# Optimization experiments

Hardware: AMD Instinct MI355X
Metric: run time of the kernel (lower is better)

## Reference

```python
import jax, jax.numpy as jnp
import numpy as np


def _gru(x_seq, W_ih, W_hh, b_ih, b_hh):
    """Batched torch-style GRU. x_seq: [B,T,H] -> outputs [B,T,H].
    Gate order (torch.nn.GRU): r, z, n. n = tanh(xn + r*(W_hn h + b_hn))."""
    B, T, H = x_seq.shape
    # precompute input projections for all timesteps: [B,T,3H]
    xp = jnp.einsum('bth,gh->btg', x_seq, W_ih) + b_ih

    def step(h, xt):  # h: [B,H], xt: [B,3H]
        hp = h @ W_hh.T + b_hh  # [B,3H]
        xr, xz, xn = jnp.split(xt, 3, axis=-1)
        hr, hz, hn = jnp.split(hp, 3, axis=-1)
        r = jax.nn.sigmoid(xr + hr)
        z = jax.nn.sigmoid(xz + hz)
        n = jnp.tanh(xn + r * hn)
        h_new = (1.0 - z) * n + z * h
        return h_new, h_new

    h0 = jnp.zeros((B, H), dtype=x_seq.dtype)
    _, hs = jax.lax.scan(step, h0, jnp.swapaxes(xp, 0, 1))  # [T,B,H]
    return jnp.swapaxes(hs, 0, 1)


def setup_inputs() -> dict:
    key = jax.random.key(0)
    B, T, C, H, D = 128, 64, 8000, 256, 16
    G = 3 * H
    ks = jax.random.split(key, 32)
    s = 0.05  # scale for stable params
    inp = {
        'x': (jax.random.uniform(ks[0], (B, T, C)) < 0.01).astype(jnp.float32),  # sparse multi-hot
        'demographic': jax.random.normal(ks[1], (B, D), jnp.float32),
        'embed_W': jax.random.normal(ks[2], (H, C), jnp.float32) * s,
        'embed_b': jax.random.normal(ks[3], (H,), jnp.float32) * s,
        'aW_ih': jax.random.normal(ks[4], (G, H), jnp.float32) * s,
        'aW_hh': jax.random.normal(ks[5], (G, H), jnp.float32) * s,
        'ab_ih': jax.random.normal(ks[6], (G,), jnp.float32) * s,
        'ab_hh': jax.random.normal(ks[7], (G,), jnp.float32) * s,
        'bW_ih': jax.random.normal(ks[8], (G, H), jnp.float32) * s,
        'bW_hh': jax.random.normal(ks[9], (G, H), jnp.float32) * s,
        'bb_ih': jax.random.normal(ks[10], (G,), jnp.float32) * s,
        'bb_hh': jax.random.normal(ks[11], (G,), jnp.float32) * s,
        'attnA_W': jax.random.normal(ks[12], (1, H), jnp.float32) * s,
        'attnA_b': jax.random.normal(ks[13], (1,), jnp.float32) * s,
        'attnB_W': jax.random.normal(ks[14], (H, H), jnp.float32) * s,
        'attnB_b': jax.random.normal(ks[15], (H,), jnp.float32) * s,
        'cls_W1': jax.random.normal(ks[16], (H, H + D), jnp.float32) * s,
        'cls_b1': jax.random.normal(ks[17], (H,), jnp.float32) * s,
        'cls_W2': jax.random.normal(ks[18], (C, H), jnp.float32) * s,
        'cls_b2': jax.random.normal(ks[19], (C,), jnp.float32) * s,
        'dl_W1': jax.random.normal(ks[20], (H, H + D), jnp.float32) * s,
        'dl_b1': jax.random.normal(ks[21], (H,), jnp.float32) * s,
        'dl_W2': jax.random.normal(ks[22], (1, H), jnp.float32) * s,
        'dl_b2': jax.random.normal(ks[23], (1,), jnp.float32) * s,
    }
    return inp


def reference(x, demographic, embed_W, embed_b,
              aW_ih, aW_hh, ab_ih, ab_hh,
              bW_ih, bW_hh, bb_ih, bb_hh,
              attnA_W, attnA_b, attnB_W, attnB_b,
              cls_W1, cls_b1, cls_W2, cls_b2,
              dl_W1, dl_b1, dl_W2, dl_b2):
    # code embedding: [B,T,C] @ [C,H] -> [B,T,H]
    embedded = jnp.einsum('btc,hc->bth', x, embed_W) + embed_b

    alpha_out = _gru(embedded, aW_ih, aW_hh, ab_ih, ab_hh)  # [B,T,H]
    beta_out = _gru(embedded, bW_ih, bW_hh, bb_ih, bb_hh)   # [B,T,H]

    e_alpha = jnp.einsum('bth,oh->bto', alpha_out, attnA_W)[..., 0] + attnA_b[0]  # [B,T]
    alpha = jax.nn.softmax(e_alpha, axis=1)                                       # [B,T]
    beta = jnp.tanh(jnp.einsum('bth,gh->btg', beta_out, attnB_W) + attnB_b)       # [B,T,H]

    context = jnp.einsum('bth,bt->bh', embedded * beta, alpha)  # [B,H]

    combined = jnp.concatenate([context, demographic], axis=1)  # [B,H+D]
    # classifier (dropout = identity, eval mode)
    h1 = jax.nn.relu(combined @ cls_W1.T + cls_b1)
    logits = h1 @ cls_W2.T + cls_b2                              # [B,C]
    # death/LOS head
    h2 = jax.nn.relu(combined @ dl_W1.T + dl_b1)
    dl_logit = h2 @ dl_W2.T + dl_b2                              # [B,1]

    return jnp.concatenate([logits, dl_logit], axis=1)          # [B,C+1]
```

## Files before the change

kernel.cpp:

```cpp
#include <hip/hip_runtime.h>


typedef __attribute__((ext_vector_type(4))) float f32x4;
typedef __attribute__((ext_vector_type(8))) short short8;

__device__ inline short f2bf(float f) {
  unsigned u = __float_as_uint(f);
  u += 0x7fffu + ((u >> 16) & 1u);
  return (short)(u >> 16);
}
__device__ inline float sigf(float x) { return 1.f / (1.f + __expf(-x)); }
__device__ inline float tanh_fast(float x) {
  x = fminf(fmaxf(x, -15.f), 15.f);
  float e = __expf(2.f * x);
  return (e - 1.f) / (e + 1.f);
}

__global__ void transpose_w(const float* __restrict__ in, float* __restrict__ outT) {
  __shared__ float tile[32][33];
  const int tx = threadIdx.x, ty = threadIdx.y;
  const int c0 = blockIdx.x * 32, h0 = blockIdx.y * 32;
#pragma unroll
  for (int k = 0; k < 4; ++k)
    tile[ty * 4 + k][tx] = in[(long)(h0 + ty * 4 + k) * 8000 + c0 + tx];
  __syncthreads();
#pragma unroll
  for (int k = 0; k < 4; ++k)
    outT[(long)(c0 + ty * 4 + k) * 256 + h0 + tx] = tile[tx][ty * 4 + k];
}

__global__ __launch_bounds__(256) void pad_w1(const float* __restrict__ w1,
                                              const float* __restrict__ w1d,
                                              float* __restrict__ o1,
                                              float* __restrict__ o2) {
  int idx = blockIdx.x * 256 + threadIdx.x;
  if (idx >= 2 * 256 * 288) return;
  int half = idx / (256 * 288);
  int r = idx % (256 * 288);
  int n = r / 288, k = r % 288;
  float v = (k < 272) ? (half ? w1d[n * 272 + k] : w1[n * 272 + k]) : 0.f;
  if (half) o2[r] = v; else o1[r] = v;
}

__global__ __launch_bounds__(512) void pack_whh(const float* __restrict__ aWhh,
                                                const float* __restrict__ bWhh,
                                                short* __restrict__ wbf) {
  const int F = blockIdx.x * 512 + threadIdx.x;
  int f = F;
  const int lane = f & 63; f >>= 6;
  const int w = f & 15; f >>= 4;
  const int e = f % 3; f /= 3;
  const int kt = f & 7; f >>= 3;
  const int gru = f;
  const float* W = gru ? bWhh : aWhh;
  const int g = e * 256 + w * 16 + (lane & 15);
  const int k = kt * 32 + (lane >> 4) * 8;
  const float* p = W + (long)g * 256 + k;
  short8 v;
#pragma unroll
  for (int j = 0; j < 8; ++j) v[j] = f2bf(p[j]);
  *(short8*)(wbf + (long)F * 8) = v;
}

__global__ __launch_bounds__(256) void embed_sparse(const float* __restrict__ x,
                                                    const float* __restrict__ Wt,
                                                    const float* __restrict__ eb,
                                                    float* __restrict__ emb) {
  __shared__ int sidx[512];
  __shared__ float sval[512];
  __shared__ int scnt;
  const int bt = blockIdx.x;
  const int tid = threadIdx.x;
  if (tid == 0) scnt = 0;
  __syncthreads();
  const float* xr = x + (long)bt * 8000;
  for (int i = tid; i < 2000; i += 256) {
    float4 v = ((const float4*)xr)[i];
    if (v.x != 0.f) { int p = atomicAdd(&scnt, 1); if (p < 512) { sidx[p] = i * 4 + 0; sval[p] = v.x; } }
    if (v.y != 0.f) { int p = atomicAdd(&scnt, 1); if (p < 512) { sidx[p] = i * 4 + 1; sval[p] = v.y; } }
    if (v.z != 0.f) { int p = atomicAdd(&scnt, 1); if (p < 512) { sidx[p] = i * 4 + 2; sval[p] = v.z; } }
    if (v.w != 0.f) { int p = atomicAdd(&scnt, 1); if (p < 512) { sidx[p] = i * 4 + 3; sval[p] = v.w; } }
  }
  __syncthreads();
  const int n = min(scnt, 512);
  float acc = eb[tid];
  for (int i = 0; i < n; ++i) acc += sval[i] * Wt[(long)sidx[i] * 256 + tid];
  emb[(long)bt * 256 + tid] = acc;
}

__global__ __launch_bounds__(256) void gemm_bt(const float* __restrict__ A,
                                               const float* __restrict__ B,
                                               const float* __restrict__ bias,
                                               float* __restrict__ C,
                                               int M, int N, int K, int ldc, int act) {
  __shared__ short As[64][40];
  __shared__ short Bs[64][40];
  const int tid = threadIdx.x;
  const int lane = tid & 63, wave = tid >> 6;
  const int wm = wave >> 1, wn = wave & 1;
  const int l15 = lane & 15, lhi = lane >> 4;
  const int m0 = blockIdx.y * 64, n0 = blockIdx.x * 64;
  const int srow = tid >> 2, scol = (tid & 3) * 8;
  f32x4 acc[2][2];
#pragma unroll
  for (int i = 0; i < 2; ++i)
#pragma unroll
    for (int j = 0; j < 2; ++j) acc[i][j] = (f32x4){0.f, 0.f, 0.f, 0.f};

  for (int k0 = 0; k0 < K; k0 += 32) {
    __syncthreads();
    {
      const float* p = A + (long)(m0 + srow) * K + k0 + scol;
      float4 f0 = *(const float4*)p;
      float4 f1 = *(const float4*)(p + 4);
      short8 v;
      v[0] = f2bf(f0.x); v[1] = f2bf(f0.y); v[2] = f2bf(f0.z); v[3] = f2bf(f0.w);
      v[4] = f2bf(f1.x); v[5] = f2bf(f1.y); v[6] = f2bf(f1.z); v[7] = f2bf(f1.w);
      *(short8*)&As[srow][scol] = v;
      const float* q = B + (long)(n0 + srow) * K + k0 + scol;
      float4 g0 = *(const float4*)q;
      float4 g1 = *(const float4*)(q + 4);
      short8 u;
      u[0] = f2bf(g0.x); u[1] = f2bf(g0.y); u[2] = f2bf(g0.z); u[3] = f2bf(g0.w);
      u[4] = f2bf(g1.x); u[5] = f2bf(g1.y); u[6] = f2bf(g1.z); u[7] = f2bf(g1.w);
      *(short8*)&Bs[srow][scol] = u;
    }
    __syncthreads();
    short8 af0 = *(const short8*)&As[wm * 32 + l15][lhi * 8];
    short8 af1 = *(const short8*)&As[wm * 32 + 16 + l15][lhi * 8];
    short8 bf0 = *(const short8*)&Bs[wn * 32 + l15][lhi * 8];
    short8 bf1 = *(const short8*)&Bs[wn * 32 + 16 + l15][lhi * 8];
    acc[0][0] = __builtin_amdgcn_mfma_f32_16x16x32_bf16(af0, bf0, acc[0][0], 0, 0, 0);
    acc[0][1] = __builtin_amdgcn_mfma_f32_16x16x32_bf16(af0, bf1, acc[0][1], 0, 0, 0);
    acc[1][0] = __builtin_amdgcn_mfma_f32_16x16x32_bf16(af1, bf0, acc[1][0], 0, 0, 0);
    acc[1][1] = __builtin_amdgcn_mfma_f32_16x16x32_bf16(af1, bf1, acc[1][1], 0, 0, 0);
  }
#pragma unroll
  for (int j = 0; j < 2; ++j) {
    const int col = n0 + wn * 32 + j * 16 + l15;
    const float bv = bias[col];
#pragma unroll
    for (int i = 0; i < 2; ++i) {
#pragma unroll
      for (int r = 0; r < 4; ++r) {
        const int row = m0 + wm * 32 + i * 16 + lhi * 4 + r;
        float v = acc[i][j][r] + bv;
        if (act == 1) v = fmaxf(v, 0.f);
        else if (act == 2) v = tanh_fast(v);
        C[(long)row * ldc + col] = v;
      }
    }
  }
}

__global__ __launch_bounds__(256) void gemm_dual(const float* __restrict__ A,
                                                 const float* __restrict__ B1,
                                                 const float* __restrict__ B2,
                                                 const float* __restrict__ bias1,
                                                 const float* __restrict__ bias2,
                                                 float* __restrict__ C1,
                                                 float* __restrict__ C2,
                                                 int K) {
  __shared__ short As[64][40];
  __shared__ short Bs1[64][40];
  __shared__ short Bs2[64][40];
  const int tid = threadIdx.x;
  const int lane = tid & 63, wave = tid >> 6;
  const int wm = wave >> 1, wn = wave & 1;
  const int l15 = lane & 15, lhi = lane >> 4;
  const int m0 = blockIdx.y * 64, n0 = blockIdx.x * 64;
  const int srow = tid >> 2, scol = (tid & 3) * 8;
  f32x4 acc1[2][2], acc2[2][2];
#pragma unroll
  for (int i = 0; i < 2; ++i)
#pragma unroll
    for (int j = 0; j < 2; ++j) {
      acc1[i][j] = (f32x4){0.f, 0.f, 0.f, 0.f};
      acc2[i][j] = (f32x4){0.f, 0.f, 0.f, 0.f};
    }

  for (int k0 = 0; k0 < K; k0 += 32) {
    __syncthreads();
    {
      const float* p = A + (long)(m0 + srow) * K + k0 + scol;
      float4 f0 = *(const float4*)p;
      float4 f1 = *(const float4*)(p + 4);
      short8 v;
      v[0] = f2bf(f0.x); v[1] = f2bf(f0.y); v[2] = f2bf(f0.z); v[3] = f2bf(f0.w);
      v[4] = f2bf(f1.x); v[5] = f2bf(f1.y); v[6] = f2bf(f1.z); v[7] = f2bf(f1.w);
      *(short8*)&As[srow][scol] = v;
      const float* q1 = B1 + (long)(n0 + srow) * K + k0 + scol;
      float4 g0 = *(const float4*)q1;
      float4 g1 = *(const float4*)(q1 + 4);
      short8 u;
      u[0] = f2bf(g0.x); u[1] = f2bf(g0.y); u[2] = f2bf(g0.z); u[3] = f2bf(g0.w);
      u[4] = f2bf(g1.x); u[5] = f2bf(g1.y); u[6] = f2bf(g1.z); u[7] = f2bf(g1.w);
      *(short8*)&Bs1[srow][scol] = u;
      const float* q2 = B2 + (long)(n0 + srow) * K + k0 + scol;
      float4 h0 = *(const float4*)q2;
      float4 h1 = *(const float4*)(q2 + 4);
      short8 t;
      t[0] = f2bf(h0.x); t[1] = f2bf(h0.y); t[2] = f2bf(h0.z); t[3] = f2bf(h0.w);
      t[4] = f2bf(h1.x); t[5] = f2bf(h1.y); t[6] = f2bf(h1.z); t[7] = f2bf(h1.w);
      *(short8*)&Bs2[srow][scol] = t;
    }
    __syncthreads();
    short8 af0 = *(const short8*)&As[wm * 32 + l15][lhi * 8];
    short8 af1 = *(const short8*)&As[wm * 32 + 16 + l15][lhi * 8];
    short8 b10 = *(const short8*)&Bs1[wn * 32 + l15][lhi * 8];
    short8 b11 = *(const short8*)&Bs1[wn * 32 + 16 + l15][lhi * 8];
    short8 b20 = *(const short8*)&Bs2[wn * 32 + l15][lhi * 8];
    short8 b21 = *(const short8*)&Bs2[wn * 32 + 16 + l15][lhi * 8];
    acc1[0][0] = __builtin_amdgcn_mfma_f32_16x16x32_bf16(af0, b10, acc1[0][0], 0, 0, 0);
    acc1[0][1] = __builtin_amdgcn_mfma_f32_16x16x32_bf16(af0, b11, acc1[0][1], 0, 0, 0);
    acc1[1][0] = __builtin_amdgcn_mfma_f32_16x16x32_bf16(af1, b10, acc1[1][0], 0, 0, 0);
    acc1[1][1] = __builtin_amdgcn_mfma_f32_16x16x32_bf16(af1, b11, acc1[1][1], 0, 0, 0);
    acc2[0][0] = __builtin_amdgcn_mfma_f32_16x16x32_bf16(af0, b20, acc2[0][0], 0, 0, 0);
    acc2[0][1] = __builtin_amdgcn_mfma_f32_16x16x32_bf16(af0, b21, acc2[0][1], 0, 0, 0);
    acc2[1][0] = __builtin_amdgcn_mfma_f32_16x16x32_bf16(af1, b20, acc2[1][0], 0, 0, 0);
    acc2[1][1] = __builtin_amdgcn_mfma_f32_16x16x32_bf16(af1, b21, acc2[1][1], 0, 0, 0);
  }
#pragma unroll
  for (int j = 0; j < 2; ++j) {
    const int col = n0 + wn * 32 + j * 16 + l15;
    const float bv1 = bias1[col];
    const float bv2 = bias2[col];
#pragma unroll
    for (int i = 0; i < 2; ++i) {
#pragma unroll
      for (int r = 0; r < 4; ++r) {
        const int row = m0 + wm * 32 + i * 16 + lhi * 4 + r;
        C1[(long)row * 768 + col] = acc1[i][j][r] + bv1;
        C2[(long)row * 768 + col] = acc2[i][j][r] + bv2;
      }
    }
  }
}

__global__ __launch_bounds__(1024, 4)
void gru_scan(const float* __restrict__ xpa,
              const float* __restrict__ xpb,
              const short* __restrict__ wbf,
              const float* __restrict__ abhh,
              const float* __restrict__ bbhh,
              float* __restrict__ aout,
              float* __restrict__ bout) {
  const int tid = threadIdx.x;
  const int lane = tid & 63, w = tid >> 6;
  const int l15 = lane & 15, lhi = lane >> 4;
  const int gru = blockIdx.x >> 5, chunk = blockIdx.x & 31;
  const int b0 = chunk * 4;
  const float* xp  = gru ? xpb : xpa;
  const float* bhh = gru ? bbhh : abhh;
  float* outp = gru ? bout : aout;

  __shared__ short hl[2][16][264];
  __shared__ float xpl[2][4][776];
  __shared__ short wlds[16][3][64][8];

  auto FR = [&](int kt, int e) -> const short8* {
    return (const short8*)(wbf + ((((long)gru * 8 + kt) * 3 + e) * 16 + w) * 512 + (long)lane * 8);
  };

  short8 wf[3][5];
#pragma unroll
  for (int e = 0; e < 3; ++e)
#pragma unroll
    for (int kt = 0; kt < 5; ++kt) wf[e][kt] = *FR(kt, e);
#pragma unroll
  for (int e = 0; e < 3; ++e) *(short8*)&wlds[w][e][lane][0] = *FR(5, e);

  float bh[3];
#pragma unroll
  for (int e = 0; e < 3; ++e) bh[e] = bhh[e * 256 + w * 16 + l15];

  for (int i = tid; i < 2 * 16 * 264; i += 1024) (&hl[0][0][0])[i] = 0;

  auto STAGE = [&](int par, int tt) {
    const int row = w / 3, seg = w % 3;
    const float* gp = xp + ((long)(b0 + row) * 64 + tt) * 768 + seg * 256 + lane * 4;
    __builtin_amdgcn_global_load_lds((const __attribute__((address_space(1))) unsigned int*)gp,
                                     (__attribute__((address_space(3))) unsigned int*)&xpl[par][row][seg * 256],
                                     16, 0, 0);
  };
  if (w < 12) STAGE(0, 0);
  __syncthreads();

  float hreg = 0.f;
  const int col = w * 16 + l15;

  for (int t = 0; t < 64; ++t) {
    const int cur = t & 1;
    short8 s60 = *FR(6, 0), s61 = *FR(6, 1), s62 = *FR(6, 2);
    short8 s70 = *FR(7, 0), s71 = *FR(7, 1), s72 = *FR(7, 2);
    if (t + 1 < 64 && w < 12) STAGE(cur ^ 1, t + 1);

    f32x4 acc[3];
#pragma unroll
    for (int e = 0; e < 3; ++e) acc[e] = (f32x4){0.f, 0.f, 0.f, 0.f};
#pragma unroll
    for (int kt = 0; kt < 5; ++kt) {
      short8 a = *(const short8*)&hl[cur][l15][kt * 32 + lhi * 8];
      acc[0] = __builtin_amdgcn_mfma_f32_16x16x32_bf16(a, wf[0][kt], acc[0], 0, 0, 0);
      acc[1] = __builtin_amdgcn_mfma_f32_16x16x32_bf16(a, wf[1][kt], acc[1], 0, 0, 0);
      acc[2] = __builtin_amdgcn_mfma_f32_16x16x32_bf16(a, wf[2][kt], acc[2], 0, 0, 0);
    }
    {
      short8 a = *(const short8*)&hl[cur][l15][5 * 32 + lhi * 8];
#pragma unroll
      for (int e = 0; e < 3; ++e) {
        short8 wl = *(const short8*)&wlds[w][e][lane][0];
        acc[e] = __builtin_amdgcn_mfma_f32_16x16x32_bf16(a, wl, acc[e], 0, 0, 0);
      }
    }
    {
      short8 a = *(const short8*)&hl[cur][l15][6 * 32 + lhi * 8];
      acc[0] = __builtin_amdgcn_mfma_f32_16x16x32_bf16(a, s60, acc[0], 0, 0, 0);
      acc[1] = __builtin_amdgcn_mfma_f32_16x16x32_bf16(a, s61, acc[1], 0, 0, 0);
      acc[2] = __builtin_amdgcn_mfma_f32_16x16x32_bf16(a, s62, acc[2], 0, 0, 0);
    }
    {
      short8 a = *(const short8*)&hl[cur][l15][7 * 32 + lhi * 8];
      acc[0] = __builtin_amdgcn_mfma_f32_16x16x32_bf16(a, s70, acc[0], 0, 0, 0);
      acc[1] = __builtin_amdgcn_mfma_f32_16x16x32_bf16(a, s71, acc[1], 0, 0, 0);
      acc[2] = __builtin_amdgcn_mfma_f32_16x16x32_bf16(a, s72, acc[2], 0, 0, 0);
    }

    {
      const float xr = xpl[cur][lhi][col];
      const float xz = xpl[cur][lhi][256 + col];
      const float xn = xpl[cur][lhi][512 + col];
      const float r = sigf(xr + acc[0][0] + bh[0]);
      const float z = sigf(xz + acc[1][0] + bh[1]);
      const float n = tanh_fast(xn + r * (acc[2][0] + bh[2]));
      const float hn = (1.f - z) * n + z * hreg;
      hreg = hn;
      hl[cur ^ 1][lhi << 2][col] = f2bf(hn);
      outp[((long)(b0 + lhi) * 64 + t) * 256 + col] = hn;
    }
    __syncthreads();
  }
}

__global__ __launch_bounds__(256) void alpha_softmax(const float* __restrict__ aout,
                                                     const float* __restrict__ aW,
                                                     const float* __restrict__ ab,
                                                     float* __restrict__ alpha) {
  __shared__ float part[64][4];
  const int b = blockIdx.x, tid = threadIdx.x;
  const int t = tid >> 2, q = tid & 3;
  const float* p = aout + (long)(b * 64 + t) * 256 + q * 64;
  const float* wv = aW + q * 64;
  float s = 0.f;
  for (int i = 0; i < 64; ++i) s += p[i] * wv[i];
  part[t][q] = s;
  __syncthreads();
  if (tid < 64) {
    float e = part[tid][0] + part[tid][1] + part[tid][2] + part[tid][3] + ab[0];
    float m = e;
    for (int k = 32; k; k >>= 1) m = fmaxf(m, __shfl_xor(m, k));
    float ex = __expf(e - m);
    float sum = ex;
    for (int k = 32; k; k >>= 1) sum += __shfl_xor(sum, k);
    alpha[b * 64 + tid] = ex / sum;
  }
}

__global__ __launch_bounds__(256) void context_combined(const float* __restrict__ alpha,
                                                        const float* __restrict__ emb,
                                                        const float* __restrict__ beta,
                                                        const float* __restrict__ demo,
                                                        float* __restrict__ comb) {
  const int b = blockIdx.x, h = threadIdx.x;
  float acc = 0.f;
  for (int t = 0; t < 64; ++t) {
    const float a = alpha[b * 64 + t];
    const long ix = (long)(b * 64 + t) * 256 + h;
    acc += a * emb[ix] * beta[ix];
  }
  comb[b * 288 + h] = acc;
  if (h < 16) comb[b * 288 + 256 + h] = demo[b * 16 + h];
  else if (h < 32) comb[b * 288 + 256 + h] = 0.f;
}

__global__ __launch_bounds__(64) void dl_head(const float* __restrict__ h2,
                                              const float* __restrict__ w,
                                              const float* __restrict__ bias,
                                              float* __restrict__ out) {
  const int b = blockIdx.x, lane = threadIdx.x;
  float s = 0.f;
#pragma unroll
  for (int i = 0; i < 4; ++i) s += h2[b * 256 + lane * 4 + i] * w[lane * 4 + i];
  for (int k = 32; k; k >>= 1) s += __shfl_xor(s, k);
  if (lane == 0) out[(long)b * 8001 + 8000] = s + bias[0];
}

extern "C" void kernel_launch(void* const* d_in, const int* in_sizes, int n_in,
                              void* d_out, int out_size, void* d_ws, size_t ws_size,
                              hipStream_t stream) {
  (void)in_sizes; (void)n_in; (void)out_size; (void)ws_size;
  const float* x      = (const float*)d_in[0];
  const float* demo   = (const float*)d_in[1];
  const float* embW   = (const float*)d_in[2];
  const float* embB   = (const float*)d_in[3];
  const float* aWih   = (const float*)d_in[4];
  const float* aWhh   = (const float*)d_in[5];
  const float* abih   = (const float*)d_in[6];
  const float* abhh   = (const float*)d_in[7];
  const float* bWih   = (const float*)d_in[8];
  const float* bWhh   = (const float*)d_in[9];
  const float* bbih   = (const float*)d_in[10];
  const float* bbhh   = (const float*)d_in[11];
  const float* attnAW = (const float*)d_in[12];
  const float* attnAb = (const float*)d_in[13];
  const float* attnBW = (const float*)d_in[14];
  const float* attnBb = (const float*)d_in[15];
  const float* clsW1  = (const float*)d_in[16];
  const float* clsb1  = (const float*)d_in[17];
  const float* clsW2  = (const float*)d_in[18];
  const float* clsb2  = (const float*)d_in[19];
  const float* dlW1   = (const float*)d_in[20];
  const float* dlb1   = (const float*)d_in[21];
  const float* dlW2   = (const float*)d_in[22];
  const float* dlb2   = (const float*)d_in[23];
  float* out = (float*)d_out;
  float* ws = (float*)d_ws;

  float* Wt    = ws;
  float* emb   = Wt + 2048000;
  float* xpa   = emb + 2097152;
  float* xpb   = xpa + 6291456;
  float* aoutB = xpb + 6291456;
  float* boutB = aoutB + 2097152;
  float* betaB = boutB + 2097152;
  float* alpha = betaB + 2097152;
  float* comb  = alpha + 8192;
  float* h1    = comb + 36864;
  float* h2    = h1 + 32768;
  float* W1p   = h2 + 32768;
  float* W1pd  = W1p + 73728;
  short* wbf   = (short*)(W1pd + 73728);

  transpose_w<<<dim3(250, 8), dim3(32, 8), 0, stream>>>(embW, Wt);
  pad_w1<<<dim3(576), dim3(256), 0, stream>>>(clsW1, dlW1, W1p, W1pd);
  pack_whh<<<dim3(96), dim3(512), 0, stream>>>(aWhh, bWhh, wbf);
  embed_sparse<<<dim3(8192), dim3(256), 0, stream>>>(x, Wt, embB, emb);
  gemm_dual<<<dim3(12, 128), dim3(256), 0, stream>>>(emb, aWih, bWih, abih, bbih, xpa, xpb, 256);
  gru_scan<<<dim3(64), dim3(1024), 0, stream>>>(xpa, xpb, wbf, abhh, bbhh, aoutB, boutB);
  alpha_softmax<<<dim3(128), dim3(256), 0, stream>>>(aoutB, attnAW, attnAb, alpha);
  gemm_bt<<<dim3(4, 128), dim3(256), 0, stream>>>(boutB, attnBW, attnBb, betaB, 8192, 256, 256, 256, 2);
  context_combined<<<dim3(128), dim3(256), 0, stream>>>(alpha, emb, betaB, demo, comb);
  gemm_bt<<<dim3(4, 2), dim3(256), 0, stream>>>(comb, W1p, clsb1, h1, 128, 256, 288, 256, 1);
  gemm_bt<<<dim3(4, 2), dim3(256), 0, stream>>>(comb, W1pd, dlb1, h2, 128, 256, 288, 256, 1);
  gemm_bt<<<dim3(125, 2), dim3(256), 0, stream>>>(h1, clsW2, clsb2, out, 128, 8000, 256, 8001, 0);
  dl_head<<<dim3(128), dim3(64), 0, stream>>>(h2, dlW2, dlb2, out);
}
```

Baseline: 279.1 us.

## Store GRU input projections in bf16 and fuse small setup/attention kernels

The gemm_dual output (input projections for both GRUs) is now written as bf16 rather than fp32, which halves that intermediate's memory traffic. gru_scan stages the bf16 rows into LDS with fewer waves and converts them back to float. pad_w1 and pack_whh are merged into one launch, and alpha_softmax is fused with context_combined, so the alpha buffer and two launches go away. The cost is reduced precision on the GRU input projections, which may shift outputs slightly.

```diff
diff --git a/kernel.cpp b/kernel.cpp
--- a/kernel.cpp
+++ b/kernel.cpp
@@ -8,6 +8,9 @@
   unsigned u = __float_as_uint(f);
   u += 0x7fffu + ((u >> 16) & 1u);
   return (short)(u >> 16);
+}
+__device__ inline float bf2f(short u) {
+  return __uint_as_float(((unsigned)(unsigned short)u) << 16);
 }
 __device__ inline float sigf(float x) { return 1.f / (1.f + __expf(-x)); }
 __device__ inline float tanh_fast(float x) {
@@ -29,37 +32,38 @@
     outT[(long)(c0 + ty * 4 + k) * 256 + h0 + tx] = tile[tx][ty * 4 + k];
 }
 
-__global__ __launch_bounds__(256) void pad_w1(const float* __restrict__ w1,
-                                              const float* __restrict__ w1d,
-                                              float* __restrict__ o1,
-                                              float* __restrict__ o2) {
-  int idx = blockIdx.x * 256 + threadIdx.x;
-  if (idx >= 2 * 256 * 288) return;
-  int half = idx / (256 * 288);
-  int r = idx % (256 * 288);
-  int n = r / 288, k = r % 288;
-  float v = (k < 272) ? (half ? w1d[n * 272 + k] : w1[n * 272 + k]) : 0.f;
-  if (half) o2[r] = v; else o1[r] = v;
-}
-
-__global__ __launch_bounds__(512) void pack_whh(const float* __restrict__ aWhh,
+__global__ __launch_bounds__(512) void pad_pack(const float* __restrict__ w1,
+                                                const float* __restrict__ w1d,
+                                                float* __restrict__ o1,
+                                                float* __restrict__ o2,
+                                                const float* __restrict__ aWhh,
                                                 const float* __restrict__ bWhh,
                                                 short* __restrict__ wbf) {
-  const int F = blockIdx.x * 512 + threadIdx.x;
-  int f = F;
-  const int lane = f & 63; f >>= 6;
-  const int w = f & 15; f >>= 4;
-  const int e = f % 3; f /= 3;
-  const int kt = f & 7; f >>= 3;
-  const int gru = f;
-  const float* W = gru ? bWhh : aWhh;
-  const int g = e * 256 + w * 16 + (lane & 15);
-  const int k = kt * 32 + (lane >> 4) * 8;
-  const float* p = W + (long)g * 256 + k;
-  short8 v;
-#pragma unroll
-  for (int j = 0; j < 8; ++j) v[j] = f2bf(p[j]);
-  *(short8*)(wbf + (long)F * 8) = v;
+  const int bid = blockIdx.x;
+  if (bid < 288) {
+    int idx = bid * 512 + threadIdx.x;
+    int half = idx / (256 * 288);
+    int r = idx % (256 * 288);
+    int n = r / 288, k = r % 288;
+    float v = (k < 272) ? (half ? w1d[n * 272 + k] : w1[n * 272 + k]) : 0.f;
+    if (half) o2[r] = v; else o1[r] = v;
+  } else {
+    const int F = (bid - 288) * 512 + threadIdx.x;
+    int f = F;
+    const int lane = f & 63; f >>= 6;
+    const int w = f & 15; f >>= 4;
+    const int e = f % 3; f /= 3;
+    const int kt = f & 7; f >>= 3;
+    const int gru = f;
+    const float* W = gru ? bWhh : aWhh;
+    const int g = e * 256 + w * 16 + (lane & 15);
+    const int k = kt * 32 + (lane >> 4) * 8;
+    const float* p = W + (long)g * 256 + k;
+    short8 v;
+#pragma unroll
+    for (int j = 0; j < 8; ++j) v[j] = f2bf(p[j]);
+    *(short8*)(wbf + (long)F * 8) = v;
+  }
 }
 
 __global__ __launch_bounds__(256) void embed_sparse(const float* __restrict__ x,
@@ -158,8 +162,8 @@
                                                  const float* __restrict__ B2,
                                                  const float* __restrict__ bias1,
                                                  const float* __restrict__ bias2,
-                                                 float* __restrict__ C1,
-                                                 float* __restrict__ C2,
+                                                 short* __restrict__ C1,
+                                                 short* __restrict__ C2,
                                                  int K) {
   __shared__ short As[64][40];
   __shared__ short Bs1[64][40];
@@ -230,16 +234,16 @@
 #pragma unroll
       for (int r = 0; r < 4; ++r) {
         const int row = m0 + wm * 32 + i * 16 + lhi * 4 + r;
-        C1[(long)row * 768 + col] = acc1[i][j][r] + bv1;
-        C2[(long)row * 768 + col] = acc2[i][j][r] + bv2;
+        C1[(long)row * 768 + col] = f2bf(acc1[i][j][r] + bv1);
+        C2[(long)row * 768 + col] = f2bf(acc2[i][j][r] + bv2);
       }
     }
   }
 }
 
 __global__ __launch_bounds__(1024, 4)
-void gru_scan(const float* __restrict__ xpa,
-              const float* __restrict__ xpb,
+void gru_scan(const short* __restrict__ xpa,
+              const short* __restrict__ xpb,
               const short* __restrict__ wbf,
               const float* __restrict__ abhh,
               const float* __restrict__ bbhh,
@@ -250,12 +254,12 @@
   const int l15 = lane & 15, lhi = lane >> 4;
   const int gru = blockIdx.x >> 5, chunk = blockIdx.x & 31;
   const int b0 = chunk * 4;
-  const float* xp  = gru ? xpb : xpa;
+  const short* xp  = gru ? xpb : xpa;
   const float* bhh = gru ? bbhh : abhh;
   float* outp = gru ? bout : aout;
 
   __shared__ short hl[2][16][264];
-  __shared__ float xpl[2][4][776];
+  __shared__ short xplb[2][4][768];
   __shared__ short wlds[16][3][64][8];
 
   auto FR = [&](int kt, int e) -> const short8* {
@@ -277,13 +281,16 @@
   for (int i = tid; i < 2 * 16 * 264; i += 1024) (&hl[0][0][0])[i] = 0;
 
   auto STAGE = [&](int par, int tt) {
-    const int row = w / 3, seg = w % 3;
-    const float* gp = xp + ((long)(b0 + row) * 64 + tt) * 768 + seg * 256 + lane * 4;
-    __builtin_amdgcn_global_load_lds((const __attribute__((address_space(1))) unsigned int*)gp,
-                                     (__attribute__((address_space(3))) unsigned int*)&xpl[par][row][seg * 256],
-                                     16, 0, 0);
+    if (w < 6) {
+      const int c = w * 64 + lane;
+      const int b = c / 96, off8 = (c % 96) * 8;
+      const short* gp = xp + ((long)(b0 + b) * 64 + tt) * 768 + off8;
+      __builtin_amdgcn_global_load_lds((const __attribute__((address_space(1))) unsigned int*)gp,
+                                       (__attribute__((address_space(3))) unsigned int*)((short*)&xplb[par][0][0] + (long)w * 512),
+                                       16, 0, 0);
+    }
   };
-  if (w < 12) STAGE(0, 0);
+  STAGE(0, 0);
   __syncthreads();
 
   float hreg = 0.f;
@@ -293,7 +300,7 @@
     const int cur = t & 1;
     short8 s60 = *FR(6, 0), s61 = *FR(6, 1), s62 = *FR(6, 2);
     short8 s70 = *FR(7, 0), s71 = *FR(7, 1), s72 = *FR(7, 2);
-    if (t + 1 < 64 && w < 12) STAGE(cur ^ 1, t + 1);
+    if (t + 1 < 64) STAGE(cur ^ 1, t + 1);
 
     f32x4 acc[3];
 #pragma unroll
@@ -327,9 +334,9 @@
     }
 
     {
-      const float xr = xpl[cur][lhi][col];
-      const float xz = xpl[cur][lhi][256 + col];
-      const float xn = xpl[cur][lhi][512 + col];
+      const float xr = bf2f(xplb[cur][lhi][col]);
+      const float xz = bf2f(xplb[cur][lhi][256 + col]);
+      const float xn = bf2f(xplb[cur][lhi][512 + col]);
       const float r = sigf(xr + acc[0][0] + bh[0]);
       const float z = sigf(xz + acc[1][0] + bh[1]);
       const float n = tanh_fast(xn + r * (acc[2][0] + bh[2]));
@@ -342,11 +349,15 @@
   }
 }
 
-__global__ __launch_bounds__(256) void alpha_softmax(const float* __restrict__ aout,
-                                                     const float* __restrict__ aW,
-                                                     const float* __restrict__ ab,
-                                                     float* __restrict__ alpha) {
+__global__ __launch_bounds__(256) void alpha_ctx(const float* __restrict__ aout,
+                                                 const float* __restrict__ aW,
+                                                 const float* __restrict__ ab,
+                                                 const float* __restrict__ emb,
+                                                 const float* __restrict__ beta,
+                                                 const float* __restrict__ demo,
+                                                 float* __restrict__ comb) {
   __shared__ float part[64][4];
+  __shared__ float al[64];
   const int b = blockIdx.x, tid = threadIdx.x;
   const int t = tid >> 2, q = tid & 3;
   const float* p = aout + (long)(b * 64 + t) * 256 + q * 64;
@@ -362,21 +373,14 @@
     float ex = __expf(e - m);
     float sum = ex;
     for (int k = 32; k; k >>= 1) sum += __shfl_xor(sum, k);
-    alpha[b * 64 + tid] = ex / sum;
-  }
-}
-
-__global__ __launch_bounds__(256) void context_combined(const float* __restrict__ alpha,
-                                                        const float* __restrict__ emb,
-                                                        const float* __restrict__ beta,
-                                                        const float* __restrict__ demo,
-                                                        float* __restrict__ comb) {
-  const int b = blockIdx.x, h = threadIdx.x;
+    al[tid] = ex / sum;
+  }
+  __syncthreads();
+  const int h = tid;
   float acc = 0.f;
-  for (int t = 0; t < 64; ++t) {
-    const float a = alpha[b * 64 + t];
-    const long ix = (long)(b * 64 + t) * 256 + h;
-    acc += a * emb[ix] * beta[ix];
+  for (int t2 = 0; t2 < 64; ++t2) {
+    const long ix = (long)(b * 64 + t2) * 256 + h;
+    acc += al[t2] * emb[ix] * beta[ix];
   }
   comb[b * 288 + h] = acc;
   if (h < 16) comb[b * 288 + 256 + h] = demo[b * 16 + h];
@@ -428,13 +432,12 @@
 
   float* Wt    = ws;
   float* emb   = Wt + 2048000;
-  float* xpa   = emb + 2097152;
-  float* xpb   = xpa + 6291456;
-  float* aoutB = xpb + 6291456;
+  short* xpa16 = (short*)(emb + 2097152);
+  short* xpb16 = xpa16 + 6291456;
+  float* aoutB = (float*)(xpb16 + 6291456);
   float* boutB = aoutB + 2097152;
   float* betaB = boutB + 2097152;
-  float* alpha = betaB + 2097152;
-  float* comb  = alpha + 8192;
+  float* comb  = betaB + 2097152;
   float* h1    = comb + 36864;
   float* h2    = h1 + 32768;
   float* W1p   = h2 + 32768;
@@ -442,14 +445,12 @@
   short* wbf   = (short*)(W1pd + 73728);
 
   transpose_w<<<dim3(250, 8), dim3(32, 8), 0, stream>>>(embW, Wt);
-  pad_w1<<<dim3(576), dim3(256), 0, stream>>>(clsW1, dlW1, W1p, W1pd);
-  pack_whh<<<dim3(96), dim3(512), 0, stream>>>(aWhh, bWhh, wbf);
+  pad_pack<<<dim3(384), dim3(512), 0, stream>>>(clsW1, dlW1, W1p, W1pd, aWhh, bWhh, wbf);
   embed_sparse<<<dim3(8192), dim3(256), 0, stream>>>(x, Wt, embB, emb);
-  gemm_dual<<<dim3(12, 128), dim3(256), 0, stream>>>(emb, aWih, bWih, abih, bbih, xpa, xpb, 256);
-  gru_scan<<<dim3(64), dim3(1024), 0, stream>>>(xpa, xpb, wbf, abhh, bbhh, aoutB, boutB);
-  alpha_softmax<<<dim3(128), dim3(256), 0, stream>>>(aoutB, attnAW, attnAb, alpha);
+  gemm_dual<<<dim3(12, 128), dim3(256), 0, stream>>>(emb, aWih, bWih, abih, bbih, xpa16, xpb16, 256);
+  gru_scan<<<dim3(64), dim3(1024), 0, stream>>>(xpa16, xpb16, wbf, abhh, bbhh, aoutB, boutB);
   gemm_bt<<<dim3(4, 128), dim3(256), 0, stream>>>(boutB, attnBW, attnBb, betaB, 8192, 256, 256, 256, 2);
-  context_combined<<<dim3(128), dim3(256), 0, stream>>>(alpha, emb, betaB, demo, comb);
+  alpha_ctx<<<dim3(128), dim3(256), 0, stream>>>(aoutB, attnAW, attnAb, emb, betaB, demo, comb);
   gemm_bt<<<dim3(4, 2), dim3(256), 0, stream>>>(comb, W1p, clsb1, h1, 128, 256, 288, 256, 1);
   gemm_bt<<<dim3(4, 2), dim3(256), 0, stream>>>(comb, W1pd, dlb1, h2, 128, 256, 288, 256, 1);
   gemm_bt<<<dim3(125, 2), dim3(256), 0, stream>>>(h1, clsW2, clsb2, out, 128, 8000, 256, 8001, 0);
```

Result: faster. 267.0 us (-4.3%).
